# Performance work log

Measured on AMD Instinct MI355X. Metric: run time of the kernel, lower is better.

## Reference

```python
import jax, jax.numpy as jnp
import numpy as np

NUM_SEG = 16
FRAMES_PER_SEG = 25
T = NUM_SEG * FRAMES_PER_SEG  # 400
PROPOSALS = jnp.array([(s, e) for s in range(NUM_SEG) for e in range(s, NUM_SEG)], dtype=jnp.int32)  # [136,2]
B, L, DV, DS, D = 16, 32, 4096, 768, 1024


def setup_inputs() -> dict:
    key = jax.random.key(0)
    ks = jax.random.split(key, 5)
    videos = jax.random.normal(ks[0], (B, T, DV), dtype=jnp.float32)
    sentences = jax.random.normal(ks[1], (B, L, DS), dtype=jnp.float32)
    Wv = jax.random.normal(ks[2], (DV, D), dtype=jnp.float32) * 0.02
    bv = jnp.zeros((D,), dtype=jnp.float32)
    Ws = jax.random.normal(ks[3], (DS, D), dtype=jnp.float32) * 0.02
    bs = jnp.zeros((D,), dtype=jnp.float32)
    idx = jax.random.randint(ks[4], (B,), 0, PROPOSALS.shape[0])
    y_true = PROPOSALS[idx]  # each ground-truth matches exactly one proposal
    return {"videos": videos, "sentences": sentences, "Wv": Wv, "bv": bv,
            "Ws": Ws, "bs": bs, "y_true": y_true}


def reference(videos, sentences, Wv, bv, Ws, bs, y_true):
    # sub-model representations (stand-ins for video_layer / sentence_layer)
    Vr = videos @ Wv + bv          # [B,T,D]
    Sr = sentences @ Ws + bs       # [B,L,D]
    # keras Attention: scores = Q @ K^T (K=V=video window), softmax over keys, out = attn @ V
    scores = jnp.einsum('bld,btd->blt', Sr, Vr)  # [B,L,T] computed once, masked per proposal
    t = jnp.arange(T)
    starts = PROPOSALS[:, 0] * FRAMES_PER_SEG
    ends = (PROPOSALS[:, 1] + 1) * FRAMES_PER_SEG
    mask = (t[None, :] >= starts[:, None]) & (t[None, :] < ends[:, None])  # [P,T]
    masked = jnp.where(mask[None, :, None, :], scores[:, None, :, :], -jnp.inf)  # [B,P,L,T]
    attn = jax.nn.softmax(masked, axis=-1)
    out = jnp.einsum('bplt,btd->bpld', attn, Vr)  # [B,P,L,D] weighted context per proposal
    # cosine_similarity along axis=0 (the L axis) -> one score vector of length D per proposal
    num = jnp.sum(out * Sr[:, None, :, :], axis=2)                     # [B,P,D]
    den = jnp.linalg.norm(out, axis=2) * jnp.linalg.norm(Sr, axis=1)[:, None, :]
    score = num / (den + 1e-15)                                        # [B,P,D]
    match = jnp.all(PROPOSALS[None, :, :] == y_true[:, None, :], axis=-1)  # [B,P]
    positive = jnp.sum(jnp.where(match[..., None], score, 0.0), axis=1)    # [B,D]
    negative = jnp.max(jnp.where(match[..., None], -jnp.inf, score), axis=(1, 2))  # [B] (tf.reduce_max over all)
    return positive, negative
```

## Files before the change

### kernel.cpp

```cpp
#include <hip/hip_runtime.h>

typedef _Float16 f16;
typedef f16 f16x4 __attribute__((ext_vector_type(4)));
typedef f16 f16x8 __attribute__((ext_vector_type(8)));
typedef float f32x4 __attribute__((ext_vector_type(4)));

__global__ void k_cast(const float* __restrict__ src, f16* __restrict__ dst, int n4) {
    int i = blockIdx.x * 256 + threadIdx.x;
    if (i < n4) {
        f32x4 v = *(const f32x4*)(src + (size_t)i * 4);
        f16x4 h = { (f16)v[0], (f16)v[1], (f16)v[2], (f16)v[3] };
        *(f16x4*)(dst + (size_t)i * 4) = h;
    }
}

__global__ __launch_bounds__(256) void k_transpose_cast(const float* __restrict__ src,
                                                        f16* __restrict__ dst, int R, int C) {
    __shared__ float tile[32 * 33];
    int tx = threadIdx.x & 31, ty = threadIdx.x >> 5;
    int c0 = blockIdx.x * 32, r0 = blockIdx.y * 32;
#pragma unroll
    for (int i = 0; i < 4; ++i) {
        int r = ty + i * 8;
        tile[r * 33 + tx] = src[(size_t)(r0 + r) * C + c0 + tx];
    }
    __syncthreads();
#pragma unroll
    for (int i = 0; i < 4; ++i) {
        int rr = ty + i * 8;
        dst[(size_t)(c0 + rr) * R + r0 + tx] = (f16)tile[tx * 33 + rr];
    }
}

__global__ __launch_bounds__(256) void k_gemm(const f16* __restrict__ A, const f16* __restrict__ Bt,
                                              const float* __restrict__ bias, float* __restrict__ C,
                                              f16* __restrict__ Ch, int M, int N, int K) {
    __shared__ f16 As[128 * 64];
    __shared__ f16 Bs[128 * 64];
    const int tid = threadIdx.x;
    const int lane = tid & 63, wave = tid >> 6;
    const int wr = wave >> 1, wc = wave & 1;
    const int m0 = blockIdx.y * 128, n0 = blockIdx.x * 128;
    const int lr = lane & 15, lq = lane >> 4;
    f32x4 acc[4][4] = {};
    for (int k0 = 0; k0 < K; k0 += 64) {
        __syncthreads();
#pragma unroll
        for (int r = 0; r < 4; ++r) {
            int o = r * 4096 + tid * 16;
            int row = o >> 7;
            int kb = (o & 127) >> 1;
            __builtin_amdgcn_global_load_lds(
                (const __attribute__((address_space(1))) void*)(A + (size_t)(m0 + row) * K + k0 + kb),
                (__attribute__((address_space(3))) void*)((char*)As + o), 16, 0, 0);
        }
#pragma unroll
        for (int r = 0; r < 4; ++r) {
            int o = r * 4096 + tid * 16;
            int row = o >> 7;
            int kb = (o & 127) >> 1;
            __builtin_amdgcn_global_load_lds(
                (const __attribute__((address_space(1))) void*)(Bt + (size_t)(n0 + row) * K + k0 + kb),
                (__attribute__((address_space(3))) void*)((char*)Bs + o), 16, 0, 0);
        }
        __syncthreads();
#pragma unroll
        for (int ks = 0; ks < 2; ++ks) {
            f16x8 af[4], bf[4];
#pragma unroll
            for (int m = 0; m < 4; ++m)
                af[m] = *(const f16x8*)&As[(wr * 64 + m * 16 + lr) * 64 + ks * 32 + lq * 8];
#pragma unroll
            for (int n = 0; n < 4; ++n)
                bf[n] = *(const f16x8*)&Bs[(wc * 64 + n * 16 + lr) * 64 + ks * 32 + lq * 8];
#pragma unroll
            for (int m = 0; m < 4; ++m)
#pragma unroll
                for (int n = 0; n < 4; ++n)
                    acc[m][n] = __builtin_amdgcn_mfma_f32_16x16x32_f16(af[m], bf[n], acc[m][n], 0, 0, 0);
        }
    }
#pragma unroll
    for (int m = 0; m < 4; ++m) {
#pragma unroll
        for (int n = 0; n < 4; ++n) {
            int col = n0 + wc * 64 + n * 16 + lr;
            float bcol = bias[col];
#pragma unroll
            for (int j = 0; j < 4; ++j) {
                int row = m0 + wr * 64 + m * 16 + lq * 4 + j;
                float v = acc[m][n][j] + bcol;
                C[(size_t)row * N + col] = v;
                Ch[(size_t)row * N + col] = (f16)v;
            }
        }
    }
}

__global__ void k_srnorm(const float* __restrict__ Sr, float* __restrict__ SrNorm) {
    int idx = blockIdx.x * 256 + threadIdx.x;
    int b = idx >> 10, d = idx & 1023;
    float s = 0.f;
#pragma unroll
    for (int l = 0; l < 32; ++l) {
        float v = Sr[((size_t)(b * 32 + l)) * 1024 + d];
        s += v * v;
    }
    SrNorm[idx] = sqrtf(s);
}

__global__ __launch_bounds__(256) void k_seg(const float* __restrict__ Vr, const f16* __restrict__ Vrh,
                                             const f16* __restrict__ Srh, float* __restrict__ W,
                                             float* __restrict__ Mg, float* __restrict__ Eg) {
    const int b = blockIdx.x >> 4, k = blockIdx.x & 15;
    __shared__ float Sm[32 * 26];
    __shared__ float P[32 * 25];
    __shared__ float VrB[25 * 260];
    const int tid = threadIdx.x;
    const int lane = tid & 63, wave = tid >> 6;
    {
        const int mf = wave >> 1, nf = wave & 1;
        const int lr = lane & 15, lq = lane >> 4;
        f32x4 acc = {};
        const f16* arow = Srh + ((size_t)(b * 32 + mf * 16 + lr)) * 1024 + lq * 8;
        const f16* brow = Vrh + ((size_t)(b * 400 + k * 25 + nf * 16 + lr)) * 1024 + lq * 8;
        for (int k0 = 0; k0 < 1024; k0 += 32) {
            f16x8 a = *(const f16x8*)(arow + k0);
            f16x8 bb = *(const f16x8*)(brow + k0);
            acc = __builtin_amdgcn_mfma_f32_16x16x32_f16(a, bb, acc, 0, 0, 0);
        }
        int t = nf * 16 + lr;
        if (t < 25) {
#pragma unroll
            for (int j = 0; j < 4; ++j) {
                int l = mf * 16 + lq * 4 + j;
                Sm[l * 26 + t] = acc[j];
            }
        }
    }
    __syncthreads();
    if (tid < 32) {
        int l = tid;
        float m = Sm[l * 26];
        for (int t = 1; t < 25; ++t) m = fmaxf(m, Sm[l * 26 + t]);
        float e = 0.f;
        for (int t = 0; t < 25; ++t) {
            float p = __expf(Sm[l * 26 + t] - m);
            P[l * 25 + t] = p;
            e += p;
        }
        Mg[(b * 16 + k) * 32 + l] = m;
        Eg[(b * 16 + k) * 32 + l] = e;
    }
    __syncthreads();
    const int dl = tid & 63, q = tid >> 6;
    for (int c = 0; c < 4; ++c) {
#pragma unroll
        for (int ii = 0; ii < 25; ++ii) {
            int idx = tid + ii * 256;
            int row = idx >> 8, dd = idx & 255;
            VrB[row * 260 + dd] = Vr[((size_t)(b * 400 + k * 25 + row)) * 1024 + c * 256 + dd];
        }
        __syncthreads();
        f32x4 accw[8] = {};
        for (int t = 0; t < 25; ++t) {
            f32x4 v = *(const f32x4*)&VrB[t * 260 + dl * 4];
#pragma unroll
            for (int li = 0; li < 8; ++li) {
                float p = P[(q + li * 4) * 25 + t];
                accw[li][0] += p * v[0];
                accw[li][1] += p * v[1];
                accw[li][2] += p * v[2];
                accw[li][3] += p * v[3];
            }
        }
#pragma unroll
        for (int li = 0; li < 8; ++li) {
            int l = q + li * 4;
            *(f32x4*)&W[(((size_t)(b * 32 + l)) * 16 + k) * 1024 + c * 256 + dl * 4] = accw[li];
        }
        __syncthreads();
    }
}

__global__ __launch_bounds__(512) void k_alpha(const float* __restrict__ Mg, const float* __restrict__ Eg,
                                               float* __restrict__ EMg, float* __restrict__ rdeng) {
    const int b = blockIdx.x;
    __shared__ float EE[32 * 16];
    __shared__ int pS[136], pE[136];
    const int tid = threadIdx.x;
    if (tid < 136) {
        int s = 0, rem = tid;
        while (rem >= 16 - s) { rem -= 16 - s; ++s; }
        pS[tid] = s;
        pE[tid] = s + rem;
    }
    if (tid < 32) {
        int l = tid;
        float G = -1e30f;
#pragma unroll
        for (int k = 0; k < 16; ++k) G = fmaxf(G, Mg[(b * 16 + k) * 32 + l]);
#pragma unroll
        for (int k = 0; k < 16; ++k) {
            float em = __expf(Mg[(b * 16 + k) * 32 + l] - G);
            EMg[((size_t)(b * 32 + l)) * 16 + k] = em;
            EE[l * 16 + k] = em * Eg[(b * 16 + k) * 32 + l];
        }
    }
    __syncthreads();
    for (int it = tid; it < 136 * 32; it += 512) {
        int p = it >> 5, l = it & 31;
        float den = 0.f;
        int s = pS[p], e = pE[p];
        for (int k = s; k <= e; ++k) den += EE[l * 16 + k];
        rdeng[((size_t)(b * 136) + p) * 32 + l] = 1.0f / (den + 1e-30f);
    }
}

__global__ __launch_bounds__(512) void k_combine(const float* __restrict__ W, const float* __restrict__ EMg,
                                                 const float* __restrict__ rdeng, const float* __restrict__ Sr,
                                                 const float* __restrict__ SrNorm, const int* __restrict__ ytrue,
                                                 float* __restrict__ out, unsigned int* __restrict__ negk) {
    extern __shared__ float v_s[];
    __shared__ float wmax_s[8];
    const int b = blockIdx.x >> 4, dc = blockIdx.x & 15;
    const int tid = threadIdx.x, lane = tid & 63, wave = tid >> 6;
    const int d = dc * 64 + lane;

#pragma unroll 4
    for (int i = 0; i < 64; ++i) {
        int idx = tid + i * 512;
        int l = idx >> 10, k = (idx >> 6) & 15;
        float em = EMg[(b * 32 + l) * 16 + k];
        v_s[idx] = W[(((size_t)(b * 32 + l)) * 16 + k) * 1024 + dc * 64 + (idx & 63)] * em;
    }
    float sr[32];
#pragma unroll
    for (int l = 0; l < 32; ++l) sr[l] = Sr[((size_t)(b * 32 + l)) * 1024 + d];
    const float srn = SrNorm[b * 1024 + d];
    const int sy = ytrue[b * 2], ey = ytrue[b * 2 + 1];
    const int pm = sy * 16 - (sy * (sy - 1)) / 2 + (ey - sy);
    __syncthreads();

    const int sA = wave, sB = 15 - wave;
    const int pA0 = sA * 16 - (sA * (sA - 1)) / 2 - sA;
    const int pB0 = sB * 16 - (sB * (sB - 1)) / 2 - sB;
    float runA[32], runB[32];
#pragma unroll
    for (int l = 0; l < 32; ++l) { runA[l] = 0.f; runB[l] = 0.f; }
    float lmax = -1e30f;

    for (int e = sA; e < 16; ++e) {
        const bool doB = (e >= sB);
        const int pA = pA0 + e, pB = pB0 + e;
        f32x4 rdA[8], rdB[8];
        const float* rA = rdeng + ((size_t)b * 136 + pA) * 32;
        const float* rB = rdeng + ((size_t)b * 136 + pB) * 32;
#pragma unroll
        for (int j = 0; j < 8; ++j) rdA[j] = *(const f32x4*)(rA + j * 4);
        if (doB) {
#pragma unroll
            for (int j = 0; j < 8; ++j) rdB[j] = *(const f32x4*)(rB + j * 4);
        }
        float numA = 0.f, ssqA = 0.f, numB = 0.f, ssqB = 0.f;
#pragma unroll
        for (int l = 0; l < 32; ++l) {
            float ve = v_s[(l * 16 + e) * 64 + lane];
            runA[l] += ve;
            float t = runA[l] * rdA[l >> 2][l & 3];
            numA += t * sr[l];
            ssqA += t * t;
            if (doB) {
                runB[l] += ve;
                float tb = runB[l] * rdB[l >> 2][l & 3];
                numB += tb * sr[l];
                ssqB += tb * tb;
            }
        }
        float scoreA = numA / (sqrtf(ssqA) * srn + 1e-15f);
        if (pA == pm) out[b * 1024 + d] = scoreA;
        else lmax = fmaxf(lmax, scoreA);
        if (doB) {
            float scoreB = numB / (sqrtf(ssqB) * srn + 1e-15f);
            if (pB == pm) out[b * 1024 + d] = scoreB;
            else lmax = fmaxf(lmax, scoreB);
        }
    }
#pragma unroll
    for (int off = 32; off >= 1; off >>= 1) lmax = fmaxf(lmax, __shfl_xor(lmax, off));
    if (lane == 0) wmax_s[wave] = lmax;
    __syncthreads();
    if (tid == 0) {
        float m = wmax_s[0];
#pragma unroll
        for (int w = 1; w < 8; ++w) m = fmaxf(m, wmax_s[w]);
        unsigned u = __float_as_uint(m);
        unsigned key = (u & 0x80000000u) ? ~u : (u | 0x80000000u);
        atomicMax(&negk[b], key);
    }
}

__global__ void k_init(unsigned* __restrict__ negk) {
    if (threadIdx.x < 16) negk[threadIdx.x] = 0u;
}

__global__ void k_negout(const unsigned* __restrict__ negk, float* __restrict__ out) {
    int i = threadIdx.x;
    if (i < 16) {
        unsigned key = negk[i];
        unsigned u = (key & 0x80000000u) ? (key ^ 0x80000000u) : ~key;
        out[16384 + i] = __uint_as_float(u);
    }
}

extern "C" void kernel_launch(void* const* d_in, const int* in_sizes, int n_in,
                              void* d_out, int out_size, void* d_ws, size_t ws_size,
                              hipStream_t stream) {
    const float* videos = (const float*)d_in[0];
    const float* sentences = (const float*)d_in[1];
    const float* Wv = (const float*)d_in[2];
    const float* bv = (const float*)d_in[3];
    const float* Ws = (const float*)d_in[4];
    const float* bs = (const float*)d_in[5];
    const int* ytrue = (const int*)d_in[6];
    float* out = (float*)d_out;

    char* ws = (char*)d_ws;
    size_t off = 0;
    auto alloc = [&](size_t bytes) {
        char* p = ws + off;
        off = (off + bytes + 255) & ~(size_t)255;
        return p;
    };
    f16* vh = (f16*)alloc(52428800);
    f16* wvt = (f16*)alloc(8388608);
    f16* sh = (f16*)alloc(786432);
    f16* wst = (f16*)alloc(1572864);
    float* Vr = (float*)alloc(26214400);
    f16* Vrh = (f16*)alloc(13107200);
    float* Sr = (float*)alloc(2097152);
    f16* Srh = (f16*)alloc(1048576);
    float* W = (float*)alloc(33554432);
    float* Mg = (float*)alloc(32768);
    float* Eg = (float*)alloc(32768);
    float* EMg = (float*)alloc(32768);
    float* rdeng = (float*)alloc(278528);
    float* SrNorm = (float*)alloc(65536);
    unsigned* negk = (unsigned*)alloc(64);
    if (off > ws_size) return;

    hipLaunchKernelGGL(k_init, dim3(1), dim3(64), 0, stream, negk);
    hipLaunchKernelGGL(k_cast, dim3(6553600 / 256), dim3(256), 0, stream, videos, vh, 6553600);
    hipLaunchKernelGGL(k_cast, dim3(98304 / 256), dim3(256), 0, stream, sentences, sh, 98304);
    hipLaunchKernelGGL(k_transpose_cast, dim3(32, 128), dim3(256), 0, stream, Wv, wvt, 4096, 1024);
    hipLaunchKernelGGL(k_transpose_cast, dim3(32, 24), dim3(256), 0, stream, Ws, wst, 768, 1024);
    hipLaunchKernelGGL(k_gemm, dim3(8, 50), dim3(256), 0, stream, vh, wvt, bv, Vr, Vrh, 6400, 1024, 4096);
    hipLaunchKernelGGL(k_gemm, dim3(8, 4), dim3(256), 0, stream, sh, wst, bs, Sr, Srh, 512, 1024, 768);
    hipLaunchKernelGGL(k_srnorm, dim3(64), dim3(256), 0, stream, Sr, SrNorm);
    hipLaunchKernelGGL(k_seg, dim3(256), dim3(256), 0, stream, Vr, Vrh, Srh, W, Mg, Eg);
    hipLaunchKernelGGL(k_alpha, dim3(16), dim3(512), 0, stream, Mg, Eg, EMg, rdeng);
    hipLaunchKernelGGL(k_combine, dim3(256), dim3(512), 131072, stream, W, EMg, rdeng, Sr, SrNorm, ytrue, out, negk);
    hipLaunchKernelGGL(k_negout, dim3(1), dim3(64), 0, stream, negk, out);
}
```

Before: 360.7 us.

## Replace video projection GEMM with pipelined direct-to-LDS kernel and drop fp32 output

Adds a dedicated 256x128-tile GEMM for the large video projection. It uses 512 threads, global_load_lds async copies into a triple-buffered XOR-swizzled LDS, priority hints around the MFMA loop, and an XCD-aware block remap. The fp32 Vr output is removed, and k_seg now reads the f16 Vrh and converts to fp32 in shared memory. This cuts GEMM global-memory stalls and the 26 MB fp32 write, at the cost of reduced precision in the attention-weighted sum and 144 KB of LDS per block.

```diff
diff --git a/kernel.cpp b/kernel.cpp
--- a/kernel.cpp
+++ b/kernel.cpp
@@ -29,6 +29,100 @@
     for (int i = 0; i < 4; ++i) {
         int rr = ty + i * 8;
         dst[(size_t)(c0 + rr) * R + r0 + tx] = (f16)tile[tx * 33 + rr];
+    }
+}
+
+__global__ __launch_bounds__(512, 2) void k_gemm2(const f16* __restrict__ A, const f16* __restrict__ Bt,
+                                                  const float* __restrict__ bias, f16* __restrict__ Ch) {
+    constexpr int K = 4096, N = 1024;
+    constexpr int BUF = 49152;
+    __shared__ __attribute__((aligned(16))) char smem[3 * BUF];
+    const int tid = threadIdx.x;
+    const int lane = tid & 63, wave = tid >> 6;
+    const int wm = wave >> 2, wn = wave & 3;
+    const int lr = lane & 15, lq = lane >> 4;
+    const int orig = blockIdx.x;
+    const int wg = (orig & 7) * 25 + (orig >> 3);
+    const int mt = wg >> 3, nt = wg & 7;
+    const int m0 = mt * 256, n0 = nt * 128;
+    const int srow = tid >> 3;
+    const int scol = ((tid & 7) ^ ((tid >> 3) & 7)) * 8;
+    const f16* aA = A + (size_t)(m0 + srow) * K + scol;
+    const f16* aB = Bt + (size_t)(n0 + srow) * K + scol;
+    constexpr int NT = K / 64;
+
+    auto stage = [&](int bb, int kt) {
+        const f16* a0 = aA + kt * 64;
+        const f16* b0 = aB + kt * 64;
+        char* la = smem + bb + tid * 16;
+#pragma unroll
+        for (int i = 0; i < 4; ++i)
+            __builtin_amdgcn_global_load_lds(
+                (const __attribute__((address_space(1))) void*)(a0 + (size_t)i * 64 * K),
+                (__attribute__((address_space(3))) void*)(la + i * 8192), 16, 0, 0);
+        char* lb = smem + bb + 32768 + tid * 16;
+#pragma unroll
+        for (int i = 0; i < 2; ++i)
+            __builtin_amdgcn_global_load_lds(
+                (const __attribute__((address_space(1))) void*)(b0 + (size_t)i * 64 * K),
+                (__attribute__((address_space(3))) void*)(lb + i * 8192), 16, 0, 0);
+    };
+
+    f32x4 acc[8][2] = {};
+    const int xa = (lr & 7) << 4;
+
+    stage(0, 0);
+    stage(BUF, 1);
+    stage(2 * BUF, 2);
+    asm volatile("s_waitcnt vmcnt(12)" ::: "memory");
+    __builtin_amdgcn_s_barrier();
+
+    int bb = 0;
+    for (int t = 0; t < NT; ++t) {
+        const char* Ab = smem + bb;
+        const char* Bb = smem + bb + 32768;
+#pragma unroll
+        for (int ks = 0; ks < 2; ++ks) {
+            const int co = (ks * 64 + lq * 16) ^ xa;
+            f16x8 bf0 = *(const f16x8*)(Bb + (wn * 32 + lr) * 128 + co);
+            f16x8 bf1 = *(const f16x8*)(Bb + (wn * 32 + 16 + lr) * 128 + co);
+            __builtin_amdgcn_s_setprio(1);
+#pragma unroll
+            for (int m = 0; m < 8; ++m) {
+                f16x8 af = *(const f16x8*)(Ab + (wm * 128 + m * 16 + lr) * 128 + co);
+                acc[m][0] = __builtin_amdgcn_mfma_f32_16x16x32_f16(af, bf0, acc[m][0], 0, 0, 0);
+                acc[m][1] = __builtin_amdgcn_mfma_f32_16x16x32_f16(af, bf1, acc[m][1], 0, 0, 0);
+            }
+            __builtin_amdgcn_s_setprio(0);
+        }
+        __builtin_amdgcn_s_barrier();
+        if (t + 3 < NT) {
+            stage(bb, t + 3);
+            asm volatile("s_waitcnt vmcnt(12)" ::: "memory");
+        } else if (t + 2 < NT) {
+            asm volatile("s_waitcnt vmcnt(6)" ::: "memory");
+        } else if (t + 1 < NT) {
+            asm volatile("s_waitcnt vmcnt(0)" ::: "memory");
+        }
+        if (t + 1 < NT) {
+            __builtin_amdgcn_s_barrier();
+            __builtin_amdgcn_sched_barrier(0);
+        }
+        bb = (bb == 2 * BUF) ? 0 : bb + BUF;
+    }
+
+#pragma unroll
+    for (int m = 0; m < 8; ++m) {
+#pragma unroll
+        for (int n = 0; n < 2; ++n) {
+            int col = n0 + wn * 32 + n * 16 + lr;
+            float bc = bias[col];
+#pragma unroll
+            for (int j = 0; j < 4; ++j) {
+                int row = m0 + wm * 128 + m * 16 + lq * 4 + j;
+                Ch[(size_t)row * N + col] = (f16)(acc[m][n][j] + bc);
+            }
+        }
     }
 }
 
@@ -109,9 +203,9 @@
     SrNorm[idx] = sqrtf(s);
 }
 
-__global__ __launch_bounds__(256) void k_seg(const float* __restrict__ Vr, const f16* __restrict__ Vrh,
-                                             const f16* __restrict__ Srh, float* __restrict__ W,
-                                             float* __restrict__ Mg, float* __restrict__ Eg) {
+__global__ __launch_bounds__(256) void k_seg(const f16* __restrict__ Vrh, const f16* __restrict__ Srh,
+                                             float* __restrict__ W, float* __restrict__ Mg,
+                                             float* __restrict__ Eg) {
     const int b = blockIdx.x >> 4, k = blockIdx.x & 15;
     __shared__ float Sm[32 * 26];
     __shared__ float P[32 * 25];
@@ -156,10 +250,14 @@
     const int dl = tid & 63, q = tid >> 6;
     for (int c = 0; c < 4; ++c) {
 #pragma unroll
-        for (int ii = 0; ii < 25; ++ii) {
-            int idx = tid + ii * 256;
-            int row = idx >> 8, dd = idx & 255;
-            VrB[row * 260 + dd] = Vr[((size_t)(b * 400 + k * 25 + row)) * 1024 + c * 256 + dd];
+        for (int ii = 0; ii < 7; ++ii) {
+            int idx4 = tid + ii * 256;
+            if (idx4 < 1600) {
+                int row = idx4 >> 6, d4 = (idx4 & 63) * 4;
+                f16x4 h = *(const f16x4*)&Vrh[((size_t)(b * 400 + k * 25 + row)) * 1024 + c * 256 + d4];
+                f32x4 f = { (float)h[0], (float)h[1], (float)h[2], (float)h[3] };
+                *(f32x4*)&VrB[row * 260 + d4] = f;
+            }
         }
         __syncthreads();
         f32x4 accw[8] = {};
@@ -336,7 +434,6 @@
     f16* wvt = (f16*)alloc(8388608);
     f16* sh = (f16*)alloc(786432);
     f16* wst = (f16*)alloc(1572864);
-    float* Vr = (float*)alloc(26214400);
     f16* Vrh = (f16*)alloc(13107200);
     float* Sr = (float*)alloc(2097152);
     f16* Srh = (f16*)alloc(1048576);
@@ -354,10 +451,10 @@
     hipLaunchKernelGGL(k_cast, dim3(98304 / 256), dim3(256), 0, stream, sentences, sh, 98304);
     hipLaunchKernelGGL(k_transpose_cast, dim3(32, 128), dim3(256), 0, stream, Wv, wvt, 4096, 1024);
     hipLaunchKernelGGL(k_transpose_cast, dim3(32, 24), dim3(256), 0, stream, Ws, wst, 768, 1024);
-    hipLaunchKernelGGL(k_gemm, dim3(8, 50), dim3(256), 0, stream, vh, wvt, bv, Vr, Vrh, 6400, 1024, 4096);
+    hipLaunchKernelGGL(k_gemm2, dim3(200), dim3(512), 0, stream, vh, wvt, bv, Vrh);
     hipLaunchKernelGGL(k_gemm, dim3(8, 4), dim3(256), 0, stream, sh, wst, bs, Sr, Srh, 512, 1024, 768);
     hipLaunchKernelGGL(k_srnorm, dim3(64), dim3(256), 0, stream, Sr, SrNorm);
-    hipLaunchKernelGGL(k_seg, dim3(256), dim3(256), 0, stream, Vr, Vrh, Srh, W, Mg, Eg);
+    hipLaunchKernelGGL(k_seg, dim3(256), dim3(256), 0, stream, Vrh, Srh, W, Mg, Eg);
     hipLaunchKernelGGL(k_alpha, dim3(16), dim3(512), 0, stream, Mg, Eg, EMg, rdeng);
     hipLaunchKernelGGL(k_combine, dim3(256), dim3(512), 131072, stream, W, EMg, rdeng, Sr, SrNorm, ytrue, out, negk);
     hipLaunchKernelGGL(k_negout, dim3(1), dim3(64), 0, stream, negk, out);
```

Result: faster. 333.7 us (-7.5%).

## Add pipelined 256x128 video GEMM with direct-to-LDS loads and drop fp32 Vr

Applied to the files above, without the earlier changes.

Replaces the generic 128x128 GEMM for the large video projection with a dedicated 512-thread kernel. It uses 256x128 tiles, double-buffered global_load_lds transfers into swizzled LDS, explicit waitcnt/barrier scheduling with MFMA priority raising, and a remapped block order for L2 locality. The GEMM now writes only the fp16 output, and k_seg rebuilds its fp32 staging tile from the fp16 copy, which removes a 26 MB fp32 write and read. The negk init kernel is folded into k_alpha. In exchange, the weighted sum in k_seg now reads fp16-rounded values, and the hand-tuned wait counts are fragile.

```diff
diff --git a/kernel.cpp b/kernel.cpp
--- a/kernel.cpp
+++ b/kernel.cpp
@@ -4,6 +4,9 @@
 typedef f16 f16x4 __attribute__((ext_vector_type(4)));
 typedef f16 f16x8 __attribute__((ext_vector_type(8)));
 typedef float f32x4 __attribute__((ext_vector_type(4)));
+
+#define LGKM0 do { asm volatile("s_waitcnt lgkmcnt(0)" ::: "memory"); __builtin_amdgcn_sched_barrier(0); } while (0)
+#define VMW(n) asm volatile("s_waitcnt vmcnt(" #n ")" ::: "memory")
 
 __global__ void k_cast(const float* __restrict__ src, f16* __restrict__ dst, int n4) {
     int i = blockIdx.x * 256 + threadIdx.x;
@@ -29,6 +32,157 @@
     for (int i = 0; i < 4; ++i) {
         int rr = ty + i * 8;
         dst[(size_t)(c0 + rr) * R + r0 + tx] = (f16)tile[tx * 33 + rr];
+    }
+}
+
+__global__ __launch_bounds__(512, 2) void k_gemm2(const f16* __restrict__ A, const f16* __restrict__ Bt,
+                                                  const float* __restrict__ bias, f16* __restrict__ Ch) {
+    constexpr int K = 4096, N = 1024, NT = 64;
+    constexpr int BUFB = 49152;
+    __shared__ __attribute__((aligned(16))) char smem[2 * BUFB];
+    const int tid = threadIdx.x;
+    const int lane = tid & 63, wave = tid >> 6;
+    const int wm = wave >> 1, wn = wave & 1;
+    const int lr = lane & 15, lq = lane >> 4;
+    const int orig = blockIdx.x;
+    const int wg = (orig & 7) * 25 + (orig >> 3);
+    const int mt = wg >> 3, nt = wg & 7;
+    const int m0 = mt * 256, n0 = nt * 128;
+
+    auto sw = [](int r) { return (r & 3) ^ ((r >> 2) & 3); };
+    const int rA0 = tid >> 2, rA1 = (tid + 512) >> 2, rB = tid >> 2;
+    const int scA0 = (((tid) & 3) ^ sw(rA0)) * 8;
+    const int scA1 = (((tid + 512) & 3) ^ sw(rA1)) * 8;
+    const int scB = ((tid & 3) ^ sw(rB)) * 8;
+    const f16* gA0 = A + (size_t)(m0 + rA0) * K + scA0;
+    const f16* gA1 = A + (size_t)(m0 + rA1) * K + scA1;
+    const f16* gB = Bt + (size_t)(n0 + rB) * K + scB;
+
+    auto issue = [&](int c, int t, int h) {
+        const int go = t * 64 + h * 32;
+        char* base = smem + c * BUFB;
+        __builtin_amdgcn_global_load_lds(
+            (const __attribute__((address_space(1))) void*)(gA0 + go),
+            (__attribute__((address_space(3))) void*)(base + h * 16384 + tid * 16), 16, 0, 0);
+        __builtin_amdgcn_global_load_lds(
+            (const __attribute__((address_space(1))) void*)(gA1 + go),
+            (__attribute__((address_space(3))) void*)(base + h * 16384 + 8192 + tid * 16), 16, 0, 0);
+        __builtin_amdgcn_global_load_lds(
+            (const __attribute__((address_space(1))) void*)(gB + go),
+            (__attribute__((address_space(3))) void*)(base + 32768 + h * 8192 + tid * 16), 16, 0, 0);
+    };
+
+    int aoff[4], boff[4];
+#pragma unroll
+    for (int m = 0; m < 4; ++m) {
+        int r = wm * 64 + m * 16 + lr;
+        aoff[m] = r * 64 + ((lq ^ sw(r)) * 16);
+    }
+#pragma unroll
+    for (int n = 0; n < 4; ++n) {
+        int r = wn * 64 + n * 16 + lr;
+        boff[n] = r * 64 + ((lq ^ sw(r)) * 16);
+    }
+
+    f32x4 acc[4][4] = {};
+
+    issue(0, 0, 0);
+    issue(0, 0, 1);
+    issue(1, 1, 0);
+    VMW(6);
+    __builtin_amdgcn_s_barrier();
+
+    for (int t = 0; t < NT; ++t) {
+        const int c = t & 1;
+        const char* ab = smem + c * BUFB;
+        const char* bb = ab + 32768;
+        f16x8 a0, a1, a2, a3, b0, b1;
+        a0 = *(const f16x8*)(ab + aoff[0]);
+        a1 = *(const f16x8*)(ab + aoff[1]);
+        a2 = *(const f16x8*)(ab + aoff[2]);
+        a3 = *(const f16x8*)(ab + aoff[3]);
+        b0 = *(const f16x8*)(bb + boff[0]);
+        b1 = *(const f16x8*)(bb + boff[1]);
+        if (t + 1 < NT) issue(c ^ 1, t + 1, 1);
+        __builtin_amdgcn_s_barrier();
+        LGKM0;
+        __builtin_amdgcn_s_setprio(1);
+        acc[0][0] = __builtin_amdgcn_mfma_f32_16x16x32_f16(a0, b0, acc[0][0], 0, 0, 0);
+        acc[1][0] = __builtin_amdgcn_mfma_f32_16x16x32_f16(a1, b0, acc[1][0], 0, 0, 0);
+        acc[2][0] = __builtin_amdgcn_mfma_f32_16x16x32_f16(a2, b0, acc[2][0], 0, 0, 0);
+        acc[3][0] = __builtin_amdgcn_mfma_f32_16x16x32_f16(a3, b0, acc[3][0], 0, 0, 0);
+        acc[0][1] = __builtin_amdgcn_mfma_f32_16x16x32_f16(a0, b1, acc[0][1], 0, 0, 0);
+        acc[1][1] = __builtin_amdgcn_mfma_f32_16x16x32_f16(a1, b1, acc[1][1], 0, 0, 0);
+        acc[2][1] = __builtin_amdgcn_mfma_f32_16x16x32_f16(a2, b1, acc[2][1], 0, 0, 0);
+        acc[3][1] = __builtin_amdgcn_mfma_f32_16x16x32_f16(a3, b1, acc[3][1], 0, 0, 0);
+        __builtin_amdgcn_s_setprio(0);
+        __builtin_amdgcn_s_barrier();
+        b0 = *(const f16x8*)(bb + boff[2]);
+        b1 = *(const f16x8*)(bb + boff[3]);
+        __builtin_amdgcn_s_barrier();
+        LGKM0;
+        __builtin_amdgcn_s_setprio(1);
+        acc[0][2] = __builtin_amdgcn_mfma_f32_16x16x32_f16(a0, b0, acc[0][2], 0, 0, 0);
+        acc[1][2] = __builtin_amdgcn_mfma_f32_16x16x32_f16(a1, b0, acc[1][2], 0, 0, 0);
+        acc[2][2] = __builtin_amdgcn_mfma_f32_16x16x32_f16(a2, b0, acc[2][2], 0, 0, 0);
+        acc[3][2] = __builtin_amdgcn_mfma_f32_16x16x32_f16(a3, b0, acc[3][2], 0, 0, 0);
+        acc[0][3] = __builtin_amdgcn_mfma_f32_16x16x32_f16(a0, b1, acc[0][3], 0, 0, 0);
+        acc[1][3] = __builtin_amdgcn_mfma_f32_16x16x32_f16(a1, b1, acc[1][3], 0, 0, 0);
+        acc[2][3] = __builtin_amdgcn_mfma_f32_16x16x32_f16(a2, b1, acc[2][3], 0, 0, 0);
+        acc[3][3] = __builtin_amdgcn_mfma_f32_16x16x32_f16(a3, b1, acc[3][3], 0, 0, 0);
+        __builtin_amdgcn_s_setprio(0);
+        if (t == NT - 1) { VMW(0); } else { VMW(6); }
+        __builtin_amdgcn_s_barrier();
+        a0 = *(const f16x8*)(ab + 16384 + aoff[0]);
+        a1 = *(const f16x8*)(ab + 16384 + aoff[1]);
+        a2 = *(const f16x8*)(ab + 16384 + aoff[2]);
+        a3 = *(const f16x8*)(ab + 16384 + aoff[3]);
+        b0 = *(const f16x8*)(bb + 8192 + boff[0]);
+        b1 = *(const f16x8*)(bb + 8192 + boff[1]);
+        if (t + 2 < NT) issue(c, t + 2, 0);
+        __builtin_amdgcn_s_barrier();
+        LGKM0;
+        __builtin_amdgcn_s_setprio(1);
+        acc[0][0] = __builtin_amdgcn_mfma_f32_16x16x32_f16(a0, b0, acc[0][0], 0, 0, 0);
+        acc[1][0] = __builtin_amdgcn_mfma_f32_16x16x32_f16(a1, b0, acc[1][0], 0, 0, 0);
+        acc[2][0] = __builtin_amdgcn_mfma_f32_16x16x32_f16(a2, b0, acc[2][0], 0, 0, 0);
+        acc[3][0] = __builtin_amdgcn_mfma_f32_16x16x32_f16(a3, b0, acc[3][0], 0, 0, 0);
+        acc[0][1] = __builtin_amdgcn_mfma_f32_16x16x32_f16(a0, b1, acc[0][1], 0, 0, 0);
+        acc[1][1] = __builtin_amdgcn_mfma_f32_16x16x32_f16(a1, b1, acc[1][1], 0, 0, 0);
+        acc[2][1] = __builtin_amdgcn_mfma_f32_16x16x32_f16(a2, b1, acc[2][1], 0, 0, 0);
+        acc[3][1] = __builtin_amdgcn_mfma_f32_16x16x32_f16(a3, b1, acc[3][1], 0, 0, 0);
+        __builtin_amdgcn_s_setprio(0);
+        __builtin_amdgcn_s_barrier();
+        b0 = *(const f16x8*)(bb + 8192 + boff[2]);
+        b1 = *(const f16x8*)(bb + 8192 + boff[3]);
+        __builtin_amdgcn_s_barrier();
+        LGKM0;
+        __builtin_amdgcn_s_setprio(1);
+        acc[0][2] = __builtin_amdgcn_mfma_f32_16x16x32_f16(a0, b0, acc[0][2], 0, 0, 0);
+        acc[1][2] = __builtin_amdgcn_mfma_f32_16x16x32_f16(a1, b0, acc[1][2], 0, 0, 0);
+        acc[2][2] = __builtin_amdgcn_mfma_f32_16x16x32_f16(a2, b0, acc[2][2], 0, 0, 0);
+        acc[3][2] = __builtin_amdgcn_mfma_f32_16x16x32_f16(a3, b0, acc[3][2], 0, 0, 0);
+        acc[0][3] = __builtin_amdgcn_mfma_f32_16x16x32_f16(a0, b1, acc[0][3], 0, 0, 0);
+        acc[1][3] = __builtin_amdgcn_mfma_f32_16x16x32_f16(a1, b1, acc[1][3], 0, 0, 0);
+        acc[2][3] = __builtin_amdgcn_mfma_f32_16x16x32_f16(a2, b1, acc[2][3], 0, 0, 0);
+        acc[3][3] = __builtin_amdgcn_mfma_f32_16x16x32_f16(a3, b1, acc[3][3], 0, 0, 0);
+        __builtin_amdgcn_s_setprio(0);
+        if (t == NT - 2) { VMW(3); } else if (t < NT - 2) { VMW(6); }
+        __builtin_amdgcn_s_barrier();
+    }
+
+#pragma unroll
+    for (int n = 0; n < 4; ++n) {
+        int col = n0 + wn * 64 + n * 16 + lr;
+        float bc = bias[col];
+#pragma unroll
+        for (int m = 0; m < 4; ++m) {
+#pragma unroll
+            for (int j = 0; j < 4; ++j) {
+                int row = m0 + wm * 64 + m * 16 + lq * 4 + j;
+                Ch[(size_t)row * N + col] = (f16)(acc[m][n][j] + bc);
+            }
+        }
     }
 }
 
@@ -109,9 +263,9 @@
     SrNorm[idx] = sqrtf(s);
 }
 
-__global__ __launch_bounds__(256) void k_seg(const float* __restrict__ Vr, const f16* __restrict__ Vrh,
-                                             const f16* __restrict__ Srh, float* __restrict__ W,
-                                             float* __restrict__ Mg, float* __restrict__ Eg) {
+__global__ __launch_bounds__(256) void k_seg(const f16* __restrict__ Vrh, const f16* __restrict__ Srh,
+                                             float* __restrict__ W, float* __restrict__ Mg,
+                                             float* __restrict__ Eg) {
     const int b = blockIdx.x >> 4, k = blockIdx.x & 15;
     __shared__ float Sm[32 * 26];
     __shared__ float P[32 * 25];
@@ -156,10 +310,14 @@
     const int dl = tid & 63, q = tid >> 6;
     for (int c = 0; c < 4; ++c) {
 #pragma unroll
-        for (int ii = 0; ii < 25; ++ii) {
-            int idx = tid + ii * 256;
-            int row = idx >> 8, dd = idx & 255;
-            VrB[row * 260 + dd] = Vr[((size_t)(b * 400 + k * 25 + row)) * 1024 + c * 256 + dd];
+        for (int ii = 0; ii < 7; ++ii) {
+            int idx4 = tid + ii * 256;
+            if (idx4 < 1600) {
+                int row = idx4 >> 6, d4 = (idx4 & 63) * 4;
+                f16x4 h = *(const f16x4*)&Vrh[((size_t)(b * 400 + k * 25 + row)) * 1024 + c * 256 + d4];
+                f32x4 f = { (float)h[0], (float)h[1], (float)h[2], (float)h[3] };
+                *(f32x4*)&VrB[row * 260 + d4] = f;
+            }
         }
         __syncthreads();
         f32x4 accw[8] = {};
@@ -184,11 +342,13 @@
 }
 
 __global__ __launch_bounds__(512) void k_alpha(const float* __restrict__ Mg, const float* __restrict__ Eg,
-                                               float* __restrict__ EMg, float* __restrict__ rdeng) {
+                                               float* __restrict__ EMg, float* __restrict__ rdeng,
+                                               unsigned int* __restrict__ negk) {
     const int b = blockIdx.x;
     __shared__ float EE[32 * 16];
     __shared__ int pS[136], pE[136];
     const int tid = threadIdx.x;
+    if (tid == 0) negk[b] = 0u;
     if (tid < 136) {
         int s = 0, rem = tid;
         while (rem >= 16 - s) { rem -= 16 - s; ++s; }
@@ -300,10 +460,6 @@
     }
 }
 
-__global__ void k_init(unsigned* __restrict__ negk) {
-    if (threadIdx.x < 16) negk[threadIdx.x] = 0u;
-}
-
 __global__ void k_negout(const unsigned* __restrict__ negk, float* __restrict__ out) {
     int i = threadIdx.x;
     if (i < 16) {
@@ -336,7 +492,6 @@
     f16* wvt = (f16*)alloc(8388608);
     f16* sh = (f16*)alloc(786432);
     f16* wst = (f16*)alloc(1572864);
-    float* Vr = (float*)alloc(26214400);
     f16* Vrh = (f16*)alloc(13107200);
     float* Sr = (float*)alloc(2097152);
     f16* Srh = (f16*)alloc(1048576);
@@ -349,16 +504,15 @@
     unsigned* negk = (unsigned*)alloc(64);
     if (off > ws_size) return;
 
-    hipLaunchKernelGGL(k_init, dim3(1), dim3(64), 0, stream, negk);
     hipLaunchKernelGGL(k_cast, dim3(6553600 / 256), dim3(256), 0, stream, videos, vh, 6553600);
     hipLaunchKernelGGL(k_cast, dim3(98304 / 256), dim3(256), 0, stream, sentences, sh, 98304);
     hipLaunchKernelGGL(k_transpose_cast, dim3(32, 128), dim3(256), 0, stream, Wv, wvt, 4096, 1024);
     hipLaunchKernelGGL(k_transpose_cast, dim3(32, 24), dim3(256), 0, stream, Ws, wst, 768, 1024);
-    hipLaunchKernelGGL(k_gemm, dim3(8, 50), dim3(256), 0, stream, vh, wvt, bv, Vr, Vrh, 6400, 1024, 4096);
+    hipLaunchKernelGGL(k_gemm2, dim3(200), dim3(512), 0, stream, vh, wvt, bv, Vrh);
     hipLaunchKernelGGL(k_gemm, dim3(8, 4), dim3(256), 0, stream, sh, wst, bs, Sr, Srh, 512, 1024, 768);
     hipLaunchKernelGGL(k_srnorm, dim3(64), dim3(256), 0, stream, Sr, SrNorm);
-    hipLaunchKernelGGL(k_seg, dim3(256), dim3(256), 0, stream, Vr, Vrh, Srh, W, Mg, Eg);
-    hipLaunchKernelGGL(k_alpha, dim3(16), dim3(512), 0, stream, Mg, Eg, EMg, rdeng);
+    hipLaunchKernelGGL(k_seg, dim3(256), dim3(256), 0, stream, Vrh, Srh, W, Mg, Eg);
+    hipLaunchKernelGGL(k_alpha, dim3(16), dim3(512), 0, stream, Mg, Eg, EMg, rdeng, negk);
     hipLaunchKernelGGL(k_combine, dim3(256), dim3(512), 131072, stream, W, EMg, rdeng, Sr, SrNorm, ytrue, out, negk);
     hipLaunchKernelGGL(k_negout, dim3(1), dim3(64), 0, stream, negk, out);
 }
```

Result: faster. 334.3 us (-7.3%).
